# Kernel tuning notes

Hardware: AMD Instinct MI355X
Metric: run time of the kernel (lower is better)

## Reference

```python
import jax, jax.numpy as jnp
import numpy as np

B, NPTS, H, O, L, PDIM, CDIM = 16, 20000, 128, 4, 6, 8, 3
K = 3  # number of learnable sine terms in Rowdy activation


def setup_inputs() -> dict:
    key = jax.random.key(0)
    ks = jax.random.split(key, 12)
    sc = lambda fan: 1.0 / np.sqrt(fan)
    return {
        "coords": jax.random.normal(ks[0], (B, NPTS, CDIM), dtype=jnp.float32),
        "sdf": jax.random.normal(ks[1], (B, NPTS, 1), dtype=jnp.float32),
        "params": jax.random.normal(ks[2], (B, PDIM), dtype=jnp.float32),
        # branch MLP: PDIM -> H (xL hidden) -> H*O
        "branch_W0": jax.random.normal(ks[3], (PDIM, H)) * sc(PDIM),
        "branch_Wr": jax.random.normal(ks[4], (L - 1, H, H)) * sc(H),
        "branch_b": jnp.zeros((L, H)),
        "branch_Wout": jax.random.normal(ks[5], (H, H * O)) * sc(H),
        "branch_bout": jnp.zeros((H * O,)),
        # trunk MLP: (CDIM+1) -> H (xL) with Rowdy activations
        "trunk_W0": jax.random.normal(ks[6], (CDIM + 1, H)) * sc(CDIM + 1),
        "trunk_Wr": jax.random.normal(ks[7], (L - 1, H, H)) * sc(H),
        "trunk_b": jnp.zeros((L, H)),
        "rowdy_a": 0.1 * jax.random.normal(ks[8], (L, K, H)),
        "final_W": jax.random.normal(ks[9], (H, H)) * sc(H),
        "final_b": jnp.zeros((H,)),
    }


def _rowdy(z, a):
    # Rowdy activation: tanh(z) + sum_k a_k * sin(k*z); a: (K, H)
    out = jnp.tanh(z)
    for k in range(a.shape[0]):
        out = out + a[k] * jnp.sin((k + 1.0) * z)
    return out


def reference(coords, sdf, params, branch_W0, branch_Wr, branch_b,
              branch_Wout, branch_bout, trunk_W0, trunk_Wr, trunk_b,
              rowdy_a, final_W, final_b):
    # ---- branch tower (records post-activation hiddens) ----
    h = jnp.tanh(params @ branch_W0 + branch_b[0])        # (B, H)
    hiddens = [h]
    for i in range(1, L):
        h = jnp.tanh(h @ branch_Wr[i - 1] + branch_b[i])
        hiddens.append(h)
    branch_out = h @ branch_Wout + branch_bout             # (B, H*O)
    # cumulative skip sums S_i = sum_{j<=i} hidden_j
    S = [hiddens[0]]
    for i in range(1, L):
        S.append(hiddens[i] + S[-1])
    # ---- trunk tower with fusion by accumulated branch features ----
    x = jnp.concatenate([coords, sdf], axis=-1)            # (B, NPTS, CDIM+1)
    for i in range(L):
        W = trunk_W0 if i == 0 else trunk_Wr[i - 1]
        x = _rowdy(x @ W + trunk_b[i], rowdy_a[i])         # (B, NPTS, H)
        x = x * S[i][:, None, :]                           # broadcast multiply
    YL = x @ final_W + final_b                             # (B, NPTS, H)
    ZL = branch_out.reshape(B, O, H)
    # sum(ZL * YL, -1) as batched contraction over H
    return jnp.einsum('boh,bnh->bno', ZL, YL)              # (B, NPTS, O)
```

## Files before the change

kernel.cpp:

```cpp
#include <hip/hip_runtime.h>
#include <hip/hip_bf16.h>
#include <stdint.h>

#define B_    16
#define NPTS_ 20000
#define H_    128
#define O_    4
#define L_    6
#define PDIM_ 8
#define K_    3

#define TPTS 64
#define TILES_PER_B ((NPTS_ + TPTS - 1) / TPTS)

typedef __attribute__((ext_vector_type(8))) short short8;
typedef __attribute__((ext_vector_type(4))) float f32x4;
typedef __attribute__((ext_vector_type(2))) uint32_t u32x2;
typedef __attribute__((ext_vector_type(4))) uint32_t u32x4;

#define FRAG(ks, pf, pl, lane) ((((((ks)*4 + (pf))*2 + (pl))*64) + (lane))*8)
#define WFRAG(jf, ks, ln) (((size_t)((jf)*4 + (ks)) * 64 + (ln)) * 8)

__device__ __forceinline__ uint32_t cvt_pk_bf16(float a, float b) {
    uint32_t d;
    asm("v_cvt_pk_bf16_f32 %0, %1, %2" : "=v"(d) : "v"(a), "v"(b));
    return d;
}
__device__ __forceinline__ float bf2f(uint16_t h) {
    return __uint_as_float(((uint32_t)h) << 16);
}
__device__ __forceinline__ uint16_t f2bf(float x) {
    uint32_t u = __float_as_uint(x);
    uint32_t r = u + 0x7FFFu + ((u >> 16) & 1u);
    return (uint16_t)(r >> 16);
}

__device__ __forceinline__ float rowdy_cf(float z, float S, float mS,
                                          float A0, float A1, float A2) {
    float e, s1, c1;
    float zl = z * 2.8853900817779268f;
    asm("v_exp_f32 %0, %1" : "=v"(e) : "v"(zl));
    float r = __builtin_amdgcn_rcpf(e + 1.f);
    float acc = fmaf(mS, r, S);
    float zs = z * 0.15915494309189535f;
    asm("v_sin_f32 %0, %1" : "=v"(s1) : "v"(zs));
    asm("v_cos_f32 %0, %1" : "=v"(c1) : "v"(zs));
    acc = fmaf(A0, s1, acc);
    acc = fmaf(A1, s1 * c1, acc);
    float t = s1 * s1;
    acc = fmaf(A2 * s1, fmaf(t, -4.f, 3.f), acc);
    return acc;
}

__device__ __forceinline__ void act_pack4_cf(const f32x4& v,
    const float4& S4, const float4& mS4, const float4& A0,
    const float4& A1, const float4& A2, u32x2& hi, u32x2& lo) {
    float x0 = rowdy_cf(v[0], S4.x, mS4.x, A0.x, A1.x, A2.x);
    float x1 = rowdy_cf(v[1], S4.y, mS4.y, A0.y, A1.y, A2.y);
    float x2 = rowdy_cf(v[2], S4.z, mS4.z, A0.z, A1.z, A2.z);
    float x3 = rowdy_cf(v[3], S4.w, mS4.w, A0.w, A1.w, A2.w);
    uint32_t d0 = cvt_pk_bf16(x0, x1);
    uint32_t d1 = cvt_pk_bf16(x2, x3);
    float r0 = x0 - __uint_as_float(d0 << 16);
    float r1 = x1 - __uint_as_float(d0 & 0xFFFF0000u);
    float r2 = x2 - __uint_as_float(d1 << 16);
    float r3 = x3 - __uint_as_float(d1 & 0xFFFF0000u);
    hi = (u32x2){d0, d1};
    lo = (u32x2){cvt_pk_bf16(r0, r1), cvt_pk_bf16(r2, r3)};
}

__global__ void prep_branch(
    const float* __restrict__ tWr,
    const float* __restrict__ params,
    const float* __restrict__ bW0, const float* __restrict__ bWr,
    const float* __restrict__ bb,  const float* __restrict__ bWout,
    const float* __restrict__ bbout,
    const float* __restrict__ fW,  const float* __restrict__ fb,
    const float* __restrict__ ra,
    uint16_t* __restrict__ WfH, uint16_t* __restrict__ WfL,
    float* __restrict__ CF, float* __restrict__ M, float* __restrict__ c0)
{
    const int blk = blockIdx.x;
    if (blk < 40) {
        const int layer = blk >> 3;
        const int wv    = (blk >> 1) & 3;
        const int jf    = blk & 1;
        const int t     = threadIdx.x;
        const int ks    = t >> 6;
        const int ln    = t & 63;
        const int j     = wv * 32 + jf * 16 + (ln & 15);
        const int kbase = ks * 32 + (ln >> 4) * 8;
        uint16_t hi[8], lo[8];
        #pragma unroll
        for (int e = 0; e < 8; ++e) {
            float w = tWr[((size_t)layer * H_ + kbase + e) * H_ + j];
            uint16_t h = f2bf(w);
            hi[e] = h;
            lo[e] = f2bf(w - bf2f(h));
        }
        size_t dst = ((size_t)((((layer * 4 + wv) * 2 + jf) * 4 + ks) * 64 + ln)) * 8;
        #pragma unroll
        for (int e = 0; e < 8; ++e) { WfH[dst + e] = hi[e]; WfL[dst + e] = lo[e]; }
        return;
    }

    const int b = blk - 40;
    const int j = threadIdx.x & 127;
    __shared__ float h[H_];
    __shared__ float zl[O_][H_];

    float z = bb[j];
    #pragma unroll
    for (int k = 0; k < PDIM_; ++k)
        z = fmaf(params[b * PDIM_ + k], bW0[k * H_ + j], z);
    float hv = tanhf(z);
    float srun = hv;
    h[j] = hv;
    {
        float* cf = CF + (size_t)(0 * B_ + b) * 4 * H_;
        cf[0 * H_ + j] = srun;
        cf[1 * H_ + j] = ra[(0 * K_ + 0) * H_ + j] * srun;
        cf[2 * H_ + j] = 2.f * ra[(0 * K_ + 1) * H_ + j] * srun;
        cf[3 * H_ + j] = ra[(0 * K_ + 2) * H_ + j] * srun;
    }

    for (int i = 1; i < L_; ++i) {
        __syncthreads();
        const float* W = bWr + (size_t)(i - 1) * H_ * H_;
        float zz = bb[i * H_ + j];
        for (int k = 0; k < H_; ++k)
            zz = fmaf(h[k], W[k * H_ + j], zz);
        __syncthreads();
        hv = tanhf(zz);
        h[j] = hv;
        srun += hv;
        float* cf = CF + (size_t)(i * B_ + b) * 4 * H_;
        cf[0 * H_ + j] = srun;
        cf[1 * H_ + j] = ra[(i * K_ + 0) * H_ + j] * srun;
        cf[2 * H_ + j] = 2.f * ra[(i * K_ + 1) * H_ + j] * srun;
        cf[3 * H_ + j] = ra[(i * K_ + 2) * H_ + j] * srun;
    }
    __syncthreads();

    #pragma unroll
    for (int o = 0; o < O_; ++o) {
        float acc = bbout[o * H_ + j];
        for (int k = 0; k < H_; ++k)
            acc = fmaf(h[k], bWout[(size_t)k * (H_ * O_) + o * H_ + j], acc);
        zl[o][j] = acc;
    }
    __syncthreads();

    float m[O_] = {0.f, 0.f, 0.f, 0.f};
    for (int hh = 0; hh < H_; ++hh) {
        float w = fW[j * H_ + hh];
        #pragma unroll
        for (int o = 0; o < O_; ++o)
            m[o] = fmaf(w, zl[o][hh], m[o]);
    }
    #pragma unroll
    for (int o = 0; o < O_; ++o)
        M[((size_t)b * H_ + j) * O_ + o] = m[o];

    if (j < O_) {
        float acc = 0.f;
        for (int hh = 0; hh < H_; ++hh)
            acc = fmaf(fb[hh], zl[j][hh], acc);
        c0[b * O_ + j] = acc;
    }
}

__global__ __launch_bounds__(256, 2) void trunk_mfma(
    const float* __restrict__ coords, const float* __restrict__ sdf,
    const float* __restrict__ tW0,    const float* __restrict__ tb,
    const float* __restrict__ CF,     const float* __restrict__ M,
    const float* __restrict__ c0,
    const uint16_t* __restrict__ WfH, const uint16_t* __restrict__ WfL,
    float* __restrict__ out)
{
    __shared__ __align__(16) uint16_t Xf[2][4 * 4 * 2 * 64 * 8];

    const int blk  = blockIdx.x;
    const int b    = blk / TILES_PER_B;
    const int tile = blk % TILES_PER_B;
    const int p0   = tile * TPTS;
    const int t    = threadIdx.x;

    {
        const int p   = t >> 2;
        const int q   = t & 3;
        const int pf  = p >> 4;
        const int p15 = p & 15;
        int pg = p0 + p;
        int pc = pg < NPTS_ ? pg : NPTS_ - 1;
        size_t gp = (size_t)b * NPTS_ + pc;
        float in0 = coords[gp * 3 + 0], in1 = coords[gp * 3 + 1];
        float in2 = coords[gp * 3 + 2], in3 = sdf[gp];
        const float* cf0 = CF + (size_t)(0 * B_ + b) * 4 * H_;
        #pragma unroll
        for (int m = 0; m < 4; ++m) {
            const int jo = q * 32 + m * 8;
            u32x2 hiA, loA, hiB, loB;
            #pragma unroll
            for (int half = 0; half < 2; ++half) {
                const int j = jo + half * 4;
                float4 w0 = *(const float4*)(tW0 + 0 * H_ + j);
                float4 w1 = *(const float4*)(tW0 + 1 * H_ + j);
                float4 w2 = *(const float4*)(tW0 + 2 * H_ + j);
                float4 w3 = *(const float4*)(tW0 + 3 * H_ + j);
                float4 bv = *(const float4*)(tb + j);
                float4 S4 = *(const float4*)(cf0 + 0 * H_ + j);
                float4 A0 = *(const float4*)(cf0 + 1 * H_ + j);
                float4 A1 = *(const float4*)(cf0 + 2 * H_ + j);
                float4 A2 = *(const float4*)(cf0 + 3 * H_ + j);
                float4 mS4 = make_float4(-2.f * S4.x, -2.f * S4.y, -2.f * S4.z, -2.f * S4.w);
                f32x4 zv;
                zv[0] = fmaf(in3, w3.x, fmaf(in2, w2.x, fmaf(in1, w1.x, fmaf(in0, w0.x, bv.x))));
                zv[1] = fmaf(in3, w3.y, fmaf(in2, w2.y, fmaf(in1, w1.y, fmaf(in0, w0.y, bv.y))));
                zv[2] = fmaf(in3, w3.z, fmaf(in2, w2.z, fmaf(in1, w1.z, fmaf(in0, w0.z, bv.z))));
                zv[3] = fmaf(in3, w3.w, fmaf(in2, w2.w, fmaf(in1, w1.w, fmaf(in0, w0.w, bv.w))));
                if (half == 0) act_pack4_cf(zv, S4, mS4, A0, A1, A2, hiA, loA);
                else           act_pack4_cf(zv, S4, mS4, A0, A1, A2, hiB, loB);
            }
            const int lane = m * 16 + p15;
            *(u32x4*)(&Xf[0][FRAG(q, pf, 0, lane)]) = (u32x4){hiA[0], hiA[1], hiB[0], hiB[1]};
            *(u32x4*)(&Xf[0][FRAG(q, pf, 1, lane)]) = (u32x4){loA[0], loA[1], loB[0], loB[1]};
        }
    }
    __syncthreads();

    const int ln    = t & 63;
    const int wv    = t >> 6;
    const int l15   = ln & 15;
    const int l4    = ln >> 4;
    const int jbase = wv * 32;
    const int l4p   = l4 >> 1;
    const int eoff  = (l4 & 1) * 4;

    for (int layer = 1; layer < L_; ++layer) {
        const uint16_t* Xc = Xf[(layer - 1) & 1];
        uint16_t*       Xn = Xf[layer & 1];
        const size_t wbase = ((size_t)((layer - 1) * 4 + wv)) * 4096;
        const uint16_t* WH = WfH + wbase;
        const uint16_t* WL = WfL + wbase;
        const float*    cf = CF + (size_t)(layer * B_ + b) * 4 * H_;

        #pragma unroll 1
        for (int jf = 0; jf < 2; ++jf) {
            const int j4 = jbase + jf * 16 + l4 * 4;
            f32x4 acc[4];
            {
                float4 bv = *(const float4*)(tb + layer * H_ + j4);
                #pragma unroll
                for (int pf = 0; pf < 4; ++pf)
                    acc[pf] = (f32x4){bv.x, bv.y, bv.z, bv.w};
            }
            #pragma unroll
            for (int ks = 0; ks < 4; ++ks) {
                short8 aH = *(const short8*)(WH + WFRAG(jf, ks, ln));
                short8 aL = *(const short8*)(WL + WFRAG(jf, ks, ln));
                #pragma unroll
                for (int pf = 0; pf < 4; ++pf) {
                    short8 bH = *(const short8*)(&Xc[FRAG(ks, pf, 0, ln)]);
                    short8 bL = *(const short8*)(&Xc[FRAG(ks, pf, 1, ln)]);
                    acc[pf] = __builtin_amdgcn_mfma_f32_16x16x32_bf16(aH, bH, acc[pf], 0, 0, 0);
                    acc[pf] = __builtin_amdgcn_mfma_f32_16x16x32_bf16(aH, bL, acc[pf], 0, 0, 0);
                    acc[pf] = __builtin_amdgcn_mfma_f32_16x16x32_bf16(aL, bH, acc[pf], 0, 0, 0);
                }
            }
            float4 S4 = *(const float4*)(cf + 0 * H_ + j4);
            float4 A0 = *(const float4*)(cf + 1 * H_ + j4);
            float4 A1 = *(const float4*)(cf + 2 * H_ + j4);
            float4 A2 = *(const float4*)(cf + 3 * H_ + j4);
            float4 mS4 = make_float4(-2.f * S4.x, -2.f * S4.y, -2.f * S4.z, -2.f * S4.w);
            const int lanep = (jf * 2 + l4p) * 16 + l15;
            #pragma unroll
            for (int pf = 0; pf < 4; ++pf) {
                u32x2 hi, lo;
                act_pack4_cf(acc[pf], S4, mS4, A0, A1, A2, hi, lo);
                *(u32x2*)(&Xn[FRAG(wv, pf, 0, lanep) + eoff]) = hi;
                *(u32x2*)(&Xn[FRAG(wv, pf, 1, lanep) + eoff]) = lo;
            }
        }
        __syncthreads();
    }

    {
        const uint16_t* Xl = Xf[(L_ - 1) & 1];
        const int p   = t >> 2;
        const int o   = t & 3;
        const int pf  = p >> 4;
        const int p15 = p & 15;
        float acc = c0[b * O_ + o];
        const float* Mb = M + (size_t)b * H_ * O_;
        #pragma unroll
        for (int ks = 0; ks < 4; ++ks) {
            #pragma unroll
            for (int m = 0; m < 4; ++m) {
                const int lane = m * 16 + p15;
                short8 h8 = *(const short8*)(&Xl[FRAG(ks, pf, 0, lane)]);
                short8 l8 = *(const short8*)(&Xl[FRAG(ks, pf, 1, lane)]);
                const int kb = ks * 32 + m * 8;
                #pragma unroll
                for (int e = 0; e < 8; ++e) {
                    float xv = bf2f((uint16_t)h8[e]) + bf2f((uint16_t)l8[e]);
                    acc = fmaf(xv, Mb[(kb + e) * O_ + o], acc);
                }
            }
        }
        int gp = p0 + p;
        if (gp < NPTS_)
            out[((size_t)b * NPTS_ + gp) * O_ + o] = acc;
    }
}

extern "C" void kernel_launch(void* const* d_in, const int* in_sizes, int n_in,
                              void* d_out, int out_size, void* d_ws, size_t ws_size,
                              hipStream_t stream) {
    const float* coords  = (const float*)d_in[0];
    const float* sdf     = (const float*)d_in[1];
    const float* params  = (const float*)d_in[2];
    const float* bW0     = (const float*)d_in[3];
    const float* bWr     = (const float*)d_in[4];
    const float* bb      = (const float*)d_in[5];
    const float* bWout   = (const float*)d_in[6];
    const float* bbout   = (const float*)d_in[7];
    const float* tW0     = (const float*)d_in[8];
    const float* tWr     = (const float*)d_in[9];
    const float* tb      = (const float*)d_in[10];
    const float* ra      = (const float*)d_in[11];
    const float* fW      = (const float*)d_in[12];
    const float* fb      = (const float*)d_in[13];
    float* out = (float*)d_out;

    float* CF = (float*)d_ws;
    float* M  = CF + (size_t)L_ * B_ * 4 * H_;
    float* c0 = M + (size_t)B_ * H_ * O_;
    uint16_t* WfH = (uint16_t*)(c0 + B_ * O_);
    uint16_t* WfL = WfH + (size_t)(L_ - 1) * H_ * H_;

    prep_branch<<<dim3(40 + B_), dim3(256), 0, stream>>>(
        tWr, params, bW0, bWr, bb, bWout, bbout, fW, fb, ra,
        WfH, WfL, CF, M, c0);
    trunk_mfma<<<dim3(B_ * TILES_PER_B), dim3(256), 0, stream>>>(
        coords, sdf, tW0, tb, CF, M, c0, WfH, WfL, out);
}
```

Before: 487.3 us.

## Give each wave its own 16-point tile and drop block-level barriers

Restructures the trunk kernel so each wavefront owns 16 points and computes all 128 output features per layer, keeping activations in a private swizzled LDS slab. This removes the __syncthreads between layers and the cross-wave exchange of activations. The weight fragment layout changes to match, occupancy is raised to 4 blocks, and the final projection uses ds_bpermute reductions. In exchange, each wave streams every weight fragment from global memory and holds 8 accumulators, which raises register pressure and weight traffic per point.

Result: faster. 476.6 us (-2.2%).

```diff
diff --git a/kernel.cpp b/kernel.cpp
--- a/kernel.cpp
+++ b/kernel.cpp
@@ -10,16 +10,16 @@
 #define PDIM_ 8
 #define K_    3
 
-#define TPTS 64
-#define TILES_PER_B ((NPTS_ + TPTS - 1) / TPTS)
+#define PTS_PER_WAVE 16
+#define NTILES (NPTS_ / PTS_PER_WAVE)
+#define NBLOCKS (B_ * NTILES / 4)
 
 typedef __attribute__((ext_vector_type(8))) short short8;
 typedef __attribute__((ext_vector_type(4))) float f32x4;
 typedef __attribute__((ext_vector_type(2))) uint32_t u32x2;
 typedef __attribute__((ext_vector_type(4))) uint32_t u32x4;
 
-#define FRAG(ks, pf, pl, lane) ((((((ks)*4 + (pf))*2 + (pl))*64) + (lane))*8)
-#define WFRAG(jf, ks, ln) (((size_t)((jf)*4 + (ks)) * 64 + (ln)) * 8)
+#define XSL(lam) ((uint32_t)(((lam)*16) ^ (((((lam)>>3)&3))<<4)))
 
 __device__ __forceinline__ uint32_t cvt_pk_bf16(float a, float b) {
     uint32_t d;
@@ -33,6 +33,13 @@
     uint32_t u = __float_as_uint(x);
     uint32_t r = u + 0x7FFFu + ((u >> 16) & 1u);
     return (uint16_t)(r >> 16);
+}
+__device__ __forceinline__ short8 mk8(uint32_t a, uint32_t b, uint32_t c, uint32_t d) {
+    u32x4 t = (u32x4){a, b, c, d};
+    return __builtin_bit_cast(short8, t);
+}
+__device__ __forceinline__ float bperm_f(int byteaddr, float v) {
+    return __int_as_float(__builtin_amdgcn_ds_bpermute(byteaddr, __float_as_int(v)));
 }
 
 __device__ __forceinline__ float rowdy_cf(float z, float S, float mS,
@@ -83,12 +90,11 @@
     const int blk = blockIdx.x;
     if (blk < 40) {
         const int layer = blk >> 3;
-        const int wv    = (blk >> 1) & 3;
-        const int jf    = blk & 1;
+        const int JF    = blk & 7;
         const int t     = threadIdx.x;
         const int ks    = t >> 6;
         const int ln    = t & 63;
-        const int j     = wv * 32 + jf * 16 + (ln & 15);
+        const int j     = JF * 16 + (ln & 15);
         const int kbase = ks * 32 + (ln >> 4) * 8;
         uint16_t hi[8], lo[8];
         #pragma unroll
@@ -98,7 +104,7 @@
             hi[e] = h;
             lo[e] = f2bf(w - bf2f(h));
         }
-        size_t dst = ((size_t)((((layer * 4 + wv) * 2 + jf) * 4 + ks) * 64 + ln)) * 8;
+        size_t dst = ((size_t)((layer * 8 + JF) * 4 + ks) * 64 + ln) * 8;
         #pragma unroll
         for (int e = 0; e < 8; ++e) { WfH[dst + e] = hi[e]; WfL[dst + e] = lo[e]; }
         return;
@@ -170,7 +176,7 @@
     }
 }
 
-__global__ __launch_bounds__(256, 2) void trunk_mfma(
+__global__ __launch_bounds__(256, 4) void trunk_mfma(
     const float* __restrict__ coords, const float* __restrict__ sdf,
     const float* __restrict__ tW0,    const float* __restrict__ tb,
     const float* __restrict__ CF,     const float* __restrict__ M,
@@ -178,139 +184,134 @@
     const uint16_t* __restrict__ WfH, const uint16_t* __restrict__ WfL,
     float* __restrict__ out)
 {
-    __shared__ __align__(16) uint16_t Xf[2][4 * 4 * 2 * 64 * 8];
-
-    const int blk  = blockIdx.x;
-    const int b    = blk / TILES_PER_B;
-    const int tile = blk % TILES_PER_B;
-    const int p0   = tile * TPTS;
-    const int t    = threadIdx.x;
+    __shared__ __align__(16) uint8_t XPK[4][8192];
+
+    const int t   = threadIdx.x;
+    const int wv  = t >> 6;
+    const int l   = t & 63;
+    const int gid = blockIdx.x * 4 + wv;
+    const int b    = gid / NTILES;
+    const int tile = gid % NTILES;
+    const int p0   = tile * PTS_PER_WAVE;
+    const int m    = l >> 4;
+    const int p15  = l & 15;
+    const int j4b  = m * 4;
+
+    uint8_t* lb = &XPK[wv][0];
+    uint8_t* pW = lb + XSL(l);
+    const int lamA = ((l & 16) << 1) | p15;
+    uint8_t* pA = lb + (uint32_t)((m >> 1) * 1024) + XSL(lamA);
+    uint8_t* pB = lb + (uint32_t)((m >> 1) * 1024) + XSL(lamA + 16);
 
     {
-        const int p   = t >> 2;
-        const int q   = t & 3;
-        const int pf  = p >> 4;
-        const int p15 = p & 15;
-        int pg = p0 + p;
-        int pc = pg < NPTS_ ? pg : NPTS_ - 1;
-        size_t gp = (size_t)b * NPTS_ + pc;
+        const size_t gp = (size_t)b * NPTS_ + p0 + p15;
         float in0 = coords[gp * 3 + 0], in1 = coords[gp * 3 + 1];
         float in2 = coords[gp * 3 + 2], in3 = sdf[gp];
-        const float* cf0 = CF + (size_t)(0 * B_ + b) * 4 * H_;
-        #pragma unroll
-        for (int m = 0; m < 4; ++m) {
-            const int jo = q * 32 + m * 8;
-            u32x2 hiA, loA, hiB, loB;
+        const float* cf0 = CF + (size_t)b * 4 * H_;
+        #pragma unroll
+        for (int JF = 0; JF < 8; ++JF) {
+            const int j4 = JF * 16 + j4b;
+            float4 w0 = *(const float4*)(tW0 + 0 * H_ + j4);
+            float4 w1 = *(const float4*)(tW0 + 1 * H_ + j4);
+            float4 w2 = *(const float4*)(tW0 + 2 * H_ + j4);
+            float4 w3 = *(const float4*)(tW0 + 3 * H_ + j4);
+            float4 bv = *(const float4*)(tb + j4);
+            f32x4 zv;
+            zv[0] = fmaf(in3, w3.x, fmaf(in2, w2.x, fmaf(in1, w1.x, fmaf(in0, w0.x, bv.x))));
+            zv[1] = fmaf(in3, w3.y, fmaf(in2, w2.y, fmaf(in1, w1.y, fmaf(in0, w0.y, bv.y))));
+            zv[2] = fmaf(in3, w3.z, fmaf(in2, w2.z, fmaf(in1, w1.z, fmaf(in0, w0.z, bv.z))));
+            zv[3] = fmaf(in3, w3.w, fmaf(in2, w2.w, fmaf(in1, w1.w, fmaf(in0, w0.w, bv.w))));
+            float4 S4 = *(const float4*)(cf0 + 0 * H_ + j4);
+            float4 A0 = *(const float4*)(cf0 + 1 * H_ + j4);
+            float4 A1 = *(const float4*)(cf0 + 2 * H_ + j4);
+            float4 A2 = *(const float4*)(cf0 + 3 * H_ + j4);
+            float4 mS4 = make_float4(-2.f * S4.x, -2.f * S4.y, -2.f * S4.z, -2.f * S4.w);
+            u32x2 hi, lo;
+            act_pack4_cf(zv, S4, mS4, A0, A1, A2, hi, lo);
+            *(u32x4*)(pW + JF * 1024) = (u32x4){hi[0], hi[1], lo[0], lo[1]};
+        }
+    }
+
+    const uint16_t* WH = WfH;
+    const uint16_t* WL = WfL;
+    #pragma unroll 1
+    for (int layer = 1; layer <= 5; ++layer) {
+        f32x4 acc[8];
+        #pragma unroll
+        for (int JF = 0; JF < 8; ++JF) {
+            float4 bv = *(const float4*)(tb + layer * H_ + JF * 16 + j4b);
+            acc[JF] = (f32x4){bv.x, bv.y, bv.z, bv.w};
+        }
+        #pragma unroll
+        for (int ks = 0; ks < 4; ++ks) {
+            u32x4 RA = *(const u32x4*)(pA + ks * 2048);
+            u32x4 RB = *(const u32x4*)(pB + ks * 2048);
+            short8 bH = mk8(RA.x, RA.y, RB.x, RB.y);
+            short8 bL = mk8(RA.z, RA.w, RB.z, RB.w);
             #pragma unroll
-            for (int half = 0; half < 2; ++half) {
-                const int j = jo + half * 4;
-                float4 w0 = *(const float4*)(tW0 + 0 * H_ + j);
-                float4 w1 = *(const float4*)(tW0 + 1 * H_ + j);
-                float4 w2 = *(const float4*)(tW0 + 2 * H_ + j);
-                float4 w3 = *(const float4*)(tW0 + 3 * H_ + j);
-                float4 bv = *(const float4*)(tb + j);
-                float4 S4 = *(const float4*)(cf0 + 0 * H_ + j);
-                float4 A0 = *(const float4*)(cf0 + 1 * H_ + j);
-                float4 A1 = *(const float4*)(cf0 + 2 * H_ + j);
-                float4 A2 = *(const float4*)(cf0 + 3 * H_ + j);
-                float4 mS4 = make_float4(-2.f * S4.x, -2.f * S4.y, -2.f * S4.z, -2.f * S4.w);
-                f32x4 zv;
-                zv[0] = fmaf(in3, w3.x, fmaf(in2, w2.x, fmaf(in1, w1.x, fmaf(in0, w0.x, bv.x))));
-                zv[1] = fmaf(in3, w3.y, fmaf(in2, w2.y, fmaf(in1, w1.y, fmaf(in0, w0.y, bv.y))));
-                zv[2] = fmaf(in3, w3.z, fmaf(in2, w2.z, fmaf(in1, w1.z, fmaf(in0, w0.z, bv.z))));
-                zv[3] = fmaf(in3, w3.w, fmaf(in2, w2.w, fmaf(in1, w1.w, fmaf(in0, w0.w, bv.w))));
-                if (half == 0) act_pack4_cf(zv, S4, mS4, A0, A1, A2, hiA, loA);
-                else           act_pack4_cf(zv, S4, mS4, A0, A1, A2, hiB, loB);
+            for (int JF = 0; JF < 8; ++JF) {
+                const size_t off = (size_t)((JF * 4 + ks) * 512) + l * 8;
+                short8 aH = *(const short8*)(WH + off);
+                short8 aL = *(const short8*)(WL + off);
+                acc[JF] = __builtin_amdgcn_mfma_f32_16x16x32_bf16(aH, bH, acc[JF], 0, 0, 0);
+                acc[JF] = __builtin_amdgcn_mfma_f32_16x16x32_bf16(aH, bL, acc[JF], 0, 0, 0);
+                acc[JF] = __builtin_amdgcn_mfma_f32_16x16x32_bf16(aL, bH, acc[JF], 0, 0, 0);
             }
-            const int lane = m * 16 + p15;
-            *(u32x4*)(&Xf[0][FRAG(q, pf, 0, lane)]) = (u32x4){hiA[0], hiA[1], hiB[0], hiB[1]};
-            *(u32x4*)(&Xf[0][FRAG(q, pf, 1, lane)]) = (u32x4){loA[0], loA[1], loB[0], loB[1]};
-        }
-    }
-    __syncthreads();
-
-    const int ln    = t & 63;
-    const int wv    = t >> 6;
-    const int l15   = ln & 15;
-    const int l4    = ln >> 4;
-    const int jbase = wv * 32;
-    const int l4p   = l4 >> 1;
-    const int eoff  = (l4 & 1) * 4;
-
-    for (int layer = 1; layer < L_; ++layer) {
-        const uint16_t* Xc = Xf[(layer - 1) & 1];
-        uint16_t*       Xn = Xf[layer & 1];
-        const size_t wbase = ((size_t)((layer - 1) * 4 + wv)) * 4096;
-        const uint16_t* WH = WfH + wbase;
-        const uint16_t* WL = WfL + wbase;
-        const float*    cf = CF + (size_t)(layer * B_ + b) * 4 * H_;
-
-        #pragma unroll 1
-        for (int jf = 0; jf < 2; ++jf) {
-            const int j4 = jbase + jf * 16 + l4 * 4;
-            f32x4 acc[4];
-            {
-                float4 bv = *(const float4*)(tb + layer * H_ + j4);
-                #pragma unroll
-                for (int pf = 0; pf < 4; ++pf)
-                    acc[pf] = (f32x4){bv.x, bv.y, bv.z, bv.w};
-            }
-            #pragma unroll
-            for (int ks = 0; ks < 4; ++ks) {
-                short8 aH = *(const short8*)(WH + WFRAG(jf, ks, ln));
-                short8 aL = *(const short8*)(WL + WFRAG(jf, ks, ln));
-                #pragma unroll
-                for (int pf = 0; pf < 4; ++pf) {
-                    short8 bH = *(const short8*)(&Xc[FRAG(ks, pf, 0, ln)]);
-                    short8 bL = *(const short8*)(&Xc[FRAG(ks, pf, 1, ln)]);
-                    acc[pf] = __builtin_amdgcn_mfma_f32_16x16x32_bf16(aH, bH, acc[pf], 0, 0, 0);
-                    acc[pf] = __builtin_amdgcn_mfma_f32_16x16x32_bf16(aH, bL, acc[pf], 0, 0, 0);
-                    acc[pf] = __builtin_amdgcn_mfma_f32_16x16x32_bf16(aL, bH, acc[pf], 0, 0, 0);
-                }
-            }
+        }
+        const float* cf = CF + (size_t)(layer * B_ + b) * 4 * H_;
+        #pragma unroll
+        for (int JF = 0; JF < 8; ++JF) {
+            const int j4 = JF * 16 + j4b;
             float4 S4 = *(const float4*)(cf + 0 * H_ + j4);
             float4 A0 = *(const float4*)(cf + 1 * H_ + j4);
             float4 A1 = *(const float4*)(cf + 2 * H_ + j4);
             float4 A2 = *(const float4*)(cf + 3 * H_ + j4);
             float4 mS4 = make_float4(-2.f * S4.x, -2.f * S4.y, -2.f * S4.z, -2.f * S4.w);
-            const int lanep = (jf * 2 + l4p) * 16 + l15;
+            u32x2 hi, lo;
+            act_pack4_cf(acc[JF], S4, mS4, A0, A1, A2, hi, lo);
+            *(u32x4*)(pW + JF * 1024) = (u32x4){hi[0], hi[1], lo[0], lo[1]};
+        }
+        WH += 8 * 2048;
+        WL += 8 * 2048;
+    }
+
+    {
+        f32x4 part = (f32x4){0.f, 0.f, 0.f, 0.f};
+        const float* Mb = M + (size_t)b * H_ * O_;
+        #pragma unroll
+        for (int ks = 0; ks < 4; ++ks) {
+            u32x4 RA = *(const u32x4*)(pA + ks * 2048);
+            u32x4 RB = *(const u32x4*)(pB + ks * 2048);
+            const int kb = ks * 32 + m * 8;
+            uint32_t hw[4] = {RA.x, RA.y, RB.x, RB.y};
+            uint32_t lw[4] = {RA.z, RA.w, RB.z, RB.w};
             #pragma unroll
-            for (int pf = 0; pf < 4; ++pf) {
-                u32x2 hi, lo;
-                act_pack4_cf(acc[pf], S4, mS4, A0, A1, A2, hi, lo);
-                *(u32x2*)(&Xn[FRAG(wv, pf, 0, lanep) + eoff]) = hi;
-                *(u32x2*)(&Xn[FRAG(wv, pf, 1, lanep) + eoff]) = lo;
+            for (int q = 0; q < 4; ++q) {
+                float xe = __uint_as_float(hw[q] << 16) + __uint_as_float(lw[q] << 16);
+                float xo = __uint_as_float(hw[q] & 0xFFFF0000u) + __uint_as_float(lw[q] & 0xFFFF0000u);
+                float4 Me = *(const float4*)(Mb + (size_t)(kb + 2 * q) * O_);
+                float4 Mo = *(const float4*)(Mb + (size_t)(kb + 2 * q + 1) * O_);
+                part[0] = fmaf(xe, Me.x, part[0]); part[0] = fmaf(xo, Mo.x, part[0]);
+                part[1] = fmaf(xe, Me.y, part[1]); part[1] = fmaf(xo, Mo.y, part[1]);
+                part[2] = fmaf(xe, Me.z, part[2]); part[2] = fmaf(xo, Mo.z, part[2]);
+                part[3] = fmaf(xe, Me.w, part[3]); part[3] = fmaf(xo, Mo.w, part[3]);
             }
         }
-        __syncthreads();
-    }
-
-    {
-        const uint16_t* Xl = Xf[(L_ - 1) & 1];
-        const int p   = t >> 2;
-        const int o   = t & 3;
-        const int pf  = p >> 4;
-        const int p15 = p & 15;
-        float acc = c0[b * O_ + o];
-        const float* Mb = M + (size_t)b * H_ * O_;
-        #pragma unroll
-        for (int ks = 0; ks < 4; ++ks) {
-            #pragma unroll
-            for (int m = 0; m < 4; ++m) {
-                const int lane = m * 16 + p15;
-                short8 h8 = *(const short8*)(&Xl[FRAG(ks, pf, 0, lane)]);
-                short8 l8 = *(const short8*)(&Xl[FRAG(ks, pf, 1, lane)]);
-                const int kb = ks * 32 + m * 8;
-                #pragma unroll
-                for (int e = 0; e < 8; ++e) {
-                    float xv = bf2f((uint16_t)h8[e]) + bf2f((uint16_t)l8[e]);
-                    acc = fmaf(xv, Mb[(kb + e) * O_ + o], acc);
-                }
-            }
-        }
-        int gp = p0 + p;
-        if (gp < NPTS_)
-            out[((size_t)b * NPTS_ + gp) * O_ + o] = acc;
+        const int a16 = (l ^ 16) << 2;
+        const int a32 = (l ^ 32) << 2;
+        #pragma unroll
+        for (int i = 0; i < 4; ++i) {
+            float v = part[i];
+            v += bperm_f(a16, v);
+            v += bperm_f(a32, v);
+            part[i] = v;
+        }
+        float4 cv = *(const float4*)(c0 + b * O_);
+        if (l < 16) {
+            float4 o4 = make_float4(part[0] + cv.x, part[1] + cv.y,
+                                    part[2] + cv.z, part[3] + cv.w);
+            *(float4*)(out + ((size_t)b * NPTS_ + p0 + l) * O_) = o4;
+        }
     }
 }
 
@@ -342,6 +343,6 @@
     prep_branch<<<dim3(40 + B_), dim3(256), 0, stream>>>(
         tWr, params, bW0, bWr, bb, bWout, bbout, fW, fb, ra,
         WfH, WfL, CF, M, c0);
-    trunk_mfma<<<dim3(B_ * TILES_PER_B), dim3(256), 0, stream>>>(
+    trunk_mfma<<<dim3(NBLOCKS), dim3(256), 0, stream>>>(
         coords, sdf, tW0, tb, CF, M, c0, WfH, WfL, out);
 }
```
